# Kernel optimization log

Hardware: AMD Instinct MI355X
Metric: run time of the kernel (lower is better)

Reference implementation:

```python
import math
import jax, jax.numpy as jnp
import numpy as np
from jax import lax


def _l2n(v, eps=1e-12):
    return v / (jnp.linalg.norm(v) + eps)


def _sn(w_bar, u, v):
    # one power iteration (as in SpectralNorm with power_iterations=1)
    h = w_bar.shape[0]
    wm = w_bar.reshape(h, -1)
    v = _l2n(wm.T @ u)
    u = _l2n(wm @ v)
    u = lax.stop_gradient(u)  # u, v are updated via .data in torch (no grad)
    v = lax.stop_gradient(v)
    sigma = u @ (wm @ v)
    return w_bar / sigma


def _conv(x, w, stride, pad):
    return lax.conv_general_dilated(
        x, w, (stride, stride), [(pad, pad), (pad, pad)],
        dimension_numbers=('NCHW', 'OIHW', 'NCHW'))


def _make_blur_kernel():
    k = jnp.array([1., 3., 3., 1.], jnp.float32)
    k2 = k[None, :] * k[:, None]
    return k2 / k2.sum()  # 4x4, sums to 1


def _blur(x, k2, pad):
    # upfirdn2d with up=1, down=1: pad then depthwise FIR filter
    C = x.shape[1]
    xp = jnp.pad(x, ((0, 0), (0, 0), (pad[0], pad[1]), (pad[0], pad[1])))
    w = jnp.tile(k2[None, None], (C, 1, 1, 1))  # [C,1,4,4]
    return lax.conv_general_dilated(
        xp, w, (1, 1), 'VALID', feature_group_count=C,
        dimension_numbers=('NCHW', 'OIHW', 'NCHW'))


def setup_inputs() -> dict:
    key = jax.random.key(0)
    ks = jax.random.split(key, 12)
    Cin, Cout = 256, 512
    x = jax.random.normal(ks[0], (16, Cin, 64, 64), jnp.float32)
    w1_bar = jax.random.normal(ks[1], (Cin, Cin, 3, 3), jnp.float32) * 0.05
    u1 = _l2n(jax.random.normal(ks[2], (Cin,), jnp.float32))
    v1 = _l2n(jax.random.normal(ks[3], (Cin * 9,), jnp.float32))
    b1 = jnp.zeros((Cin,), jnp.float32)
    w2_bar = jax.random.normal(ks[4], (Cout, Cin, 3, 3), jnp.float32) * 0.05
    u2 = _l2n(jax.random.normal(ks[5], (Cout,), jnp.float32))
    v2 = _l2n(jax.random.normal(ks[6], (Cin * 9,), jnp.float32))
    b2 = jnp.zeros((Cout,), jnp.float32)
    ws_bar = jax.random.normal(ks[7], (Cout, Cin, 1, 1), jnp.float32) * 0.05
    us = _l2n(jax.random.normal(ks[8], (Cout,), jnp.float32))
    vs = _l2n(jax.random.normal(ks[9], (Cin,), jnp.float32))
    return dict(x=x, w1_bar=w1_bar, u1=u1, v1=v1, b1=b1,
                w2_bar=w2_bar, u2=u2, v2=v2, b2=b2,
                ws_bar=ws_bar, us=us, vs=vs)


def reference(x, w1_bar, u1, v1, b1, w2_bar, u2, v2, b2, ws_bar, us, vs):
    k2 = _make_blur_kernel()
    # conv1: 3x3 same-res, SN conv + bias + LeakyReLU(0.2)
    out = _conv(x, _sn(w1_bar, u1, v1), 1, 1) + b1[None, :, None, None]
    out = jax.nn.leaky_relu(out, 0.2)
    # conv2: blur pad=(2,2) then 3x3 stride-2 SN conv + bias + LeakyReLU
    out = _blur(out, k2, (2, 2))
    out = _conv(out, _sn(w2_bar, u2, v2), 2, 0) + b2[None, :, None, None]
    out = jax.nn.leaky_relu(out, 0.2)
    # skip: blur pad=(1,1) then 1x1 stride-2 SN conv (no bias, no act)
    skip = _blur(x, k2, (1, 1))
    skip = _conv(skip, _sn(ws_bar, us, vs), 2, 0)
    return (out + skip) / math.sqrt(2)
```

## Files before the change

### kernel.cpp

```cpp
#include <hip/hip_runtime.h>
#include <math.h>

typedef unsigned short u16;
typedef __attribute__((ext_vector_type(8))) unsigned short ushort8;
typedef __attribute__((ext_vector_type(4))) unsigned short u16x4;
typedef __attribute__((ext_vector_type(8))) short short8;
typedef __attribute__((ext_vector_type(4))) float f32x4;

__device__ __forceinline__ float b2f(u16 v) {
    unsigned u = ((unsigned)v) << 16; float f; __builtin_memcpy(&f, &u, 4); return f;
}
__device__ __forceinline__ u16 f2b(float f) {
    unsigned u; __builtin_memcpy(&u, &f, 4);
    u = (u + 0x7fffu + ((u >> 16) & 1u)) >> 16;
    return (u16)u;
}
__device__ __forceinline__ float ldin(const void* p, int i, int flag) {
    return flag ? ((const float*)p)[i] : b2f(((const u16*)p)[i]);
}
__device__ __forceinline__ void split2(float x, u16& h, u16& l) {
    h = f2b(x);
    l = f2b(x - b2f(h));
}
__device__ __forceinline__ ushort8 zero8() {
    ushort8 z;
#pragma unroll
    for (int i = 0; i < 8; ++i) z[i] = 0;
    return z;
}
__device__ __forceinline__ void tile_barrier() {
    asm volatile("s_waitcnt lgkmcnt(0)" ::: "memory");
    __builtin_amdgcn_s_barrier();
    asm volatile("" ::: "memory");
}

__global__ void detect_kernel(const unsigned* __restrict__ xw, int* __restrict__ flag) {
    __shared__ int red[4];
    int tid = threadIdx.x, lane = tid & 63, wid = tid >> 6;
    int cnt = 0;
    for (int i = 0; i < 16; ++i) {
        unsigned w = xw[tid * 16 + i];
        unsigned e = (w >> 23) & 0xFF;
        if (e >= 77u && e <= 157u) ++cnt;
    }
    for (int o = 32; o; o >>= 1) cnt += __shfl_down(cnt, o, 64);
    if (lane == 0) red[wid] = cnt;
    __syncthreads();
    if (tid == 0) flag[0] = (red[0] + red[1] + red[2] + red[3] >= 2048) ? 1 : 0;
}

__global__ void sig_init_kernel(float* __restrict__ t, float* __restrict__ ns) {
    int i = blockIdx.x * 256 + threadIdx.x;
    if (i < 4864) t[i] = 0.f;
    if (i < 3) ns[i] = 0.f;
}

__global__ void sig_t_kernel(const void* __restrict__ w1, const void* __restrict__ u1,
                             const void* __restrict__ w2, const void* __restrict__ u2,
                             const void* __restrict__ wsb, const void* __restrict__ us,
                             const int* __restrict__ flagp, float* __restrict__ t) {
    __shared__ float ush[64];
    int blk = blockIdx.x;
    int flag = flagp[0];
    const void* W; const void* U; int m, toff, jc, ic;
    if (blk < 36)       { W = w1;  U = u1; m = 2304; toff = 0;    jc = blk % 9; ic = blk / 9; }
    else if (blk < 108) { int r = blk - 36;  W = w2;  U = u2; m = 2304; toff = 2304; jc = r % 9; ic = r / 9; }
    else                { int r = blk - 108; W = wsb; U = us; m = 256;  toff = 4608; jc = 0;     ic = r; }
    int tid = threadIdx.x;
    if (tid < 64) ush[tid] = ldin(U, ic * 64 + tid, flag);
    __syncthreads();
    int j = jc * 256 + tid;
    float acc = 0.f;
    int base = ic * 64 * m + j;
    for (int ii = 0; ii < 64; ++ii) acc += ldin(W, base + ii * m, flag) * ush[ii];
    atomicAdd(&t[toff + j], acc);
}

__global__ void sig_norm_kernel(float* __restrict__ t, float* __restrict__ ntinv) {
    __shared__ float red[4];
    int b = blockIdx.x;
    int m = (b == 2) ? 256 : 2304;
    int toff = b * 2304;
    int tid = threadIdx.x, lane = tid & 63, wid = tid >> 6;
    float s = 0.f;
    for (int j = tid; j < m; j += 256) { float v = t[toff + j]; s += v * v; }
    for (int o = 32; o; o >>= 1) s += __shfl_down(s, o, 64);
    if (lane == 0) red[wid] = s;
    __syncthreads();
    if (tid == 0) ntinv[b] = 1.f / (sqrtf(red[0] + red[1] + red[2] + red[3]) + 1e-12f);
}

__global__ void sig_s_kernel(const void* __restrict__ w1, const void* __restrict__ w2,
                             const void* __restrict__ wsb, const int* __restrict__ flagp,
                             const float* __restrict__ t, const float* __restrict__ ntinv,
                             float* __restrict__ ns) {
    int flag = flagp[0];
    int wg = blockIdx.x * 4 + (threadIdx.x >> 6);
    int lane = threadIdx.x & 63;
    const void* W; int m, toff, i, b;
    if (wg < 256)      { W = w1;  m = 2304; toff = 0;    i = wg;       b = 0; }
    else if (wg < 768) { W = w2;  m = 2304; toff = 2304; i = wg - 256; b = 1; }
    else               { W = wsb; m = 256;  toff = 4608; i = wg - 768; b = 2; }
    float acc = 0.f;
    int base = i * m;
    for (int j = lane; j < m; j += 64) acc += ldin(W, base + j, flag) * t[toff + j];
    for (int o = 32; o; o >>= 1) acc += __shfl_down(acc, o, 64);
    if (lane == 0) { float s = acc * ntinv[b]; atomicAdd(&ns[b], s * s); }
}

__global__ void sig_fin_kernel(const float* __restrict__ ns, float* __restrict__ inv_sigma) {
    int b = threadIdx.x;
    if (b < 3) { float s2 = ns[b]; float s = sqrtf(s2); inv_sigma[b] = (s + 1e-12f) / s2; }
}

__global__ void wprep_kernel(const void* __restrict__ w1b, const void* __restrict__ w2b,
                             const void* __restrict__ wsb,
                             const void* __restrict__ b1,  const void* __restrict__ b2,
                             const float* __restrict__ inv_sigma, const int* __restrict__ flagp,
                             u16* __restrict__ w1h, u16* __restrict__ w1l,
                             u16* __restrict__ w2h, u16* __restrict__ w2l,
                             u16* __restrict__ wsh, u16* __restrict__ wsl,
                             float* __restrict__ b1f, float* __restrict__ b2f_) {
    int idx = blockIdx.x * 256 + threadIdx.x;
    int flag = flagp[0];
    float s0 = inv_sigma[0], s1 = inv_sigma[1], s2 = inv_sigma[2];
    if (idx < 589824) {
        int kyx = idx / 65536; int rem = idx - kyx * 65536;
        int co = rem >> 8, ci = rem & 255;
        float w = ldin(w1b, ((co << 8) + ci) * 9 + kyx, flag) * s0;
        split2(w, w1h[idx], w1l[idx]);
    } else if (idx < 589824 + 1179648) {
        int i2 = idx - 589824;
        int kyx = i2 / 131072; int rem = i2 - kyx * 131072;
        int co = rem >> 8, ci = rem & 255;
        float w = ldin(w2b, ((co << 8) + ci) * 9 + kyx, flag) * s1;
        split2(w, w2h[i2], w2l[i2]);
    } else if (idx < 1900544) {
        int i3 = idx - 1769472;
        float w = ldin(wsb, i3, flag) * s2;
        split2(w, wsh[i3], wsl[i3]);
    } else if (idx < 1900544 + 256) {
        b1f[idx - 1900544] = ldin(b1, idx - 1900544, flag);
    } else if (idx < 1900544 + 768) {
        b2f_[idx - 1900800] = ldin(b2, idx - 1900800, flag);
    }
}

__global__ void transpose_kernel(const void* __restrict__ x, u16* __restrict__ xh,
                                 u16* __restrict__ xl,
                                 const int* __restrict__ flagp, int n0) {
    __shared__ float tile[32][65];
    int flag = flagp[0];
    int ny  = blockIdx.x;
    int ci0 = blockIdx.y * 32;
    int nl = ny >> 6, y = ny & 63;
    int t = threadIdx.x;
    int ci_l = t >> 3, x8 = (t & 7) * 8;
    int base = ((n0 + nl) * 256 + ci0 + ci_l) * 4096 + y * 64 + x8;
#pragma unroll
    for (int k = 0; k < 8; ++k) tile[ci_l][x8 + k] = ldin(x, base + k, flag);
    __syncthreads();
    int x_l = t >> 2, oc = (t & 3) * 8;
    size_t o = ((size_t)ny * 64 + x_l) * 256 + ci0 + oc;
    ushort8 h, l;
#pragma unroll
    for (int k = 0; k < 8; ++k) {
        u16 hh, ll; split2(tile[oc + k][x_l], hh, ll);
        h[k] = hh; l[k] = ll;
    }
    *(ushort8*)&xh[o] = h;
    *(ushort8*)&xl[o] = l;
}

__device__ __constant__ float BW[4] = {0.125f, 0.375f, 0.375f, 0.125f};

__global__ void blur1_kernel(const u16* __restrict__ a1h, const u16* __restrict__ a1l,
                             u16* __restrict__ bh, u16* __restrict__ bl) {
    int idx = blockIdx.x * 256 + threadIdx.x;
    int q = (idx & 63) * 4;
    int rem = idx >> 6;
    int xq = rem % 65; rem /= 65;
    int yq = rem % 65;
    int n  = rem / 65;
    float4 acc = {0.f, 0.f, 0.f, 0.f};
#pragma unroll
    for (int i = 0; i < 4; ++i) {
        int yy = yq + i - 2;
        if ((unsigned)yy >= 64u) continue;
#pragma unroll
        for (int j = 0; j < 4; ++j) {
            int xx = xq + j - 2;
            if ((unsigned)xx >= 64u) continue;
            float w = BW[i] * BW[j];
            size_t g = ((size_t)((n * 64 + yy) * 64 + xx) << 8) + q;
            u16x4 vh = *(const u16x4*)&a1h[g];
            u16x4 vl = *(const u16x4*)&a1l[g];
            acc.x += w * (b2f(vh[0]) + b2f(vl[0]));
            acc.y += w * (b2f(vh[1]) + b2f(vl[1]));
            acc.z += w * (b2f(vh[2]) + b2f(vl[2]));
            acc.w += w * (b2f(vh[3]) + b2f(vl[3]));
        }
    }
    u16x4 h, l;
    u16 hh, ll;
    split2(acc.x, hh, ll); h[0] = hh; l[0] = ll;
    split2(acc.y, hh, ll); h[1] = hh; l[1] = ll;
    split2(acc.z, hh, ll); h[2] = hh; l[2] = ll;
    split2(acc.w, hh, ll); h[3] = hh; l[3] = ll;
    *(u16x4*)&bh[(size_t)idx * 4] = h;
    *(u16x4*)&bl[(size_t)idx * 4] = l;
}

__global__ void blursample_kernel(const u16* __restrict__ xh, const u16* __restrict__ xl,
                                  u16* __restrict__ sh, u16* __restrict__ sl) {
    int idx = blockIdx.x * 256 + threadIdx.x;
    int q = (idx & 63) * 4;
    int rem = idx >> 6;
    int xo = rem & 31;
    int yo = (rem >> 5) & 31;
    int n  = rem >> 10;
    float4 acc = {0.f, 0.f, 0.f, 0.f};
#pragma unroll
    for (int i = 0; i < 4; ++i) {
        int yy = 2 * yo + i - 1;
        if ((unsigned)yy >= 64u) continue;
#pragma unroll
        for (int j = 0; j < 4; ++j) {
            int xx = 2 * xo + j - 1;
            if ((unsigned)xx >= 64u) continue;
            float w = BW[i] * BW[j];
            size_t g = ((size_t)((n * 64 + yy) * 64 + xx) << 8) + q;
            u16x4 vh = *(const u16x4*)&xh[g];
            u16x4 vl = *(const u16x4*)&xl[g];
            acc.x += w * (b2f(vh[0]) + b2f(vl[0]));
            acc.y += w * (b2f(vh[1]) + b2f(vl[1]));
            acc.z += w * (b2f(vh[2]) + b2f(vl[2]));
            acc.w += w * (b2f(vh[3]) + b2f(vl[3]));
        }
    }
    u16x4 h, l;
    u16 hh, ll;
    split2(acc.x, hh, ll); h[0] = hh; l[0] = ll;
    split2(acc.y, hh, ll); h[1] = hh; l[1] = ll;
    split2(acc.z, hh, ll); h[2] = hh; l[2] = ll;
    split2(acc.w, hh, ll); h[3] = hh; l[3] = ll;
    *(u16x4*)&sh[(size_t)idx * 4] = h;
    *(u16x4*)&sl[(size_t)idx * 4] = l;
}

#define LDK 40

#define C1_LOAD(IT, RAH0, RAH1, RAL0, RAL1, RBH0, RBH1, RBL0, RBL1) {          \
    int p_ = (IT) >> 3, kc_ = (IT) & 7;                                        \
    const u16* wh_ = w1h + (size_t)p_ * 65536;                                 \
    const u16* wl_ = w1l + (size_t)p_ * 65536;                                 \
    size_t gs_ = (size_t)(co_base + ra) * 256 + kc_ * 32 + ka;                 \
    RAH0 = *(const ushort8*)&wh_[gs_];                                         \
    RAH1 = *(const ushort8*)&wh_[gs_ + 8];                                     \
    if (DOLO) { RAL0 = *(const ushort8*)&wl_[gs_];                             \
                RAL1 = *(const ushort8*)&wl_[gs_ + 8]; }                       \
    int dy_ = p_ / 3 - 1, dx_ = p_ % 3 - 1;                                    \
    int yy_ = y0 + (ra >> 6) + dy_, xx_ = (ra & 63) + dx_;                     \
    if ((unsigned)yy_ < 64u && (unsigned)xx_ < 64u) {                          \
        size_t g_ = ((size_t)((n * 64 + yy_) * 64 + xx_) << 8) + kc_ * 32 + ka;\
        RBH0 = *(const ushort8*)&xh[g_];                                       \
        RBH1 = *(const ushort8*)&xh[g_ + 8];                                   \
        if (DOLO) { RBL0 = *(const ushort8*)&xl[g_];                           \
                    RBL1 = *(const ushort8*)&xl[g_ + 8]; }                     \
    } else {                                                                   \
        RBH0 = zero8(); RBH1 = zero8();                                        \
        if (DOLO) { RBL0 = zero8(); RBL1 = zero8(); }                          \
    }                                                                          \
}

template <bool DOLO>
__device__ __forceinline__ void conv1_body(
        const u16* __restrict__ xh, const u16* __restrict__ xl,
        const u16* __restrict__ w1h, const u16* __restrict__ w1l,
        const float* __restrict__ b1f, u16* __restrict__ a1h, u16* __restrict__ a1l,
        u16* Ah, u16* Al, u16* Bh, u16* Bl) {
    int tid = threadIdx.x, lane = tid & 63, wid = tid >> 6;
    int col = lane & 15, quad = lane >> 4;
    int wco = (wid >> 1) * 64, wsp = (wid & 1) * 64;
    int bidx = blockIdx.x;
    int sp_blk = (bidx & 7) * 32 + (bidx >> 3);
    int sp_base = sp_blk * 128;
    int co_base = blockIdx.y * 128;
    int n  = sp_base >> 12;
    int y0 = (sp_base & 4095) >> 6;
    int ra = tid >> 1, ka = (tid & 1) * 16;

    f32x4 acc[4][4];
#pragma unroll
    for (int i = 0; i < 4; ++i)
#pragma unroll
        for (int j = 0; j < 4; ++j) acc[i][j] = (f32x4){0.f, 0.f, 0.f, 0.f};

    ushort8 nAh0, nAh1, nAl0, nAl1, nBh0, nBh1, nBl0, nBl1;
    C1_LOAD(0, nAh0, nAh1, nAl0, nAl1, nBh0, nBh1, nBl0, nBl1);

    for (int it = 0; it < 72; ++it) {
        __syncthreads();
        *(ushort8*)&Ah[ra * LDK + ka]     = nAh0;
        *(ushort8*)&Ah[ra * LDK + ka + 8] = nAh1;
        if (DOLO) {
            *(ushort8*)&Al[ra * LDK + ka]     = nAl0;
            *(ushort8*)&Al[ra * LDK + ka + 8] = nAl1;
        }
        *(ushort8*)&Bh[ra * LDK + ka]     = nBh0;
        *(ushort8*)&Bh[ra * LDK + ka + 8] = nBh1;
        if (DOLO) {
            *(ushort8*)&Bl[ra * LDK + ka]     = nBl0;
            *(ushort8*)&Bl[ra * LDK + ka + 8] = nBl1;
        }
        int itn = (it + 1 < 72) ? it + 1 : it;
        C1_LOAD(itn, nAh0, nAh1, nAl0, nAl1, nBh0, nBh1, nBl0, nBl1);
        tile_barrier();
        short8 ah[4], al[4];
#pragma unroll
        for (int tm = 0; tm < 4; ++tm) {
            ah[tm] = *(const short8*)&Ah[(wco + tm * 16 + col) * LDK + quad * 8];
            if (DOLO) al[tm] = *(const short8*)&Al[(wco + tm * 16 + col) * LDK + quad * 8];
        }
#pragma unroll
        for (int tn = 0; tn < 4; ++tn) {
            short8 bh = *(const short8*)&Bh[(wsp + tn * 16 + col) * LDK + quad * 8];
            short8 bl;
            if (DOLO) bl = *(const short8*)&Bl[(wsp + tn * 16 + col) * LDK + quad * 8];
#pragma unroll
            for (int tm = 0; tm < 4; ++tm) {
                acc[tm][tn] = __builtin_amdgcn_mfma_f32_16x16x32_bf16(ah[tm], bh, acc[tm][tn], 0, 0, 0);
                if (DOLO) {
                    acc[tm][tn] = __builtin_amdgcn_mfma_f32_16x16x32_bf16(ah[tm], bl, acc[tm][tn], 0, 0, 0);
                    acc[tm][tn] = __builtin_amdgcn_mfma_f32_16x16x32_bf16(al[tm], bh, acc[tm][tn], 0, 0, 0);
                }
            }
        }
    }
#pragma unroll
    for (int tm = 0; tm < 4; ++tm) {
        int cog = co_base + wco + tm * 16 + quad * 4;
        float4 bias = *(const float4*)&b1f[cog];
        float bb[4] = {bias.x, bias.y, bias.z, bias.w};
#pragma unroll
        for (int tn = 0; tn < 4; ++tn) {
            int sp = sp_base + wsp + tn * 16 + col;
            u16x4 oh, ol;
#pragma unroll
            for (int r = 0; r < 4; ++r) {
                float v = acc[tm][tn][r] + bb[r];
                v = v > 0.f ? v : 0.2f * v;
                u16 hh, ll; split2(v, hh, ll);
                oh[r] = hh; ol[r] = ll;
            }
            *(u16x4*)&a1h[((size_t)sp << 8) + cog] = oh;
            *(u16x4*)&a1l[((size_t)sp << 8) + cog] = ol;
        }
    }
}

__global__ __launch_bounds__(256, 2) void conv1_kernel(
        const u16* __restrict__ xh, const u16* __restrict__ xl,
        const u16* __restrict__ w1h, const u16* __restrict__ w1l,
        const float* __restrict__ b1f, u16* __restrict__ a1h, u16* __restrict__ a1l,
        const int* __restrict__ flagp) {
    __shared__ u16 Ah[128 * LDK];
    __shared__ u16 Al[128 * LDK];
    __shared__ u16 Bh[128 * LDK];
    __shared__ u16 Bl[128 * LDK];
    if (flagp[0]) conv1_body<true >(xh, xl, w1h, w1l, b1f, a1h, a1l, Ah, Al, Bh, Bl);
    else          conv1_body<false>(xh, xl, w1h, w1l, b1f, a1h, a1l, Ah, Al, Bh, Bl);
}

#define C2_LOAD(IT, RAH, RAL, RBH0, RBH1, RBL0, RBL1) {                        \
    int p_ = (IT) >> 3, kc_ = (IT) & 7; int ci0_ = kc_ * 32;                   \
    const u16* wh_ = (p_ < 9) ? w2h + (size_t)p_ * 131072 : wsh;               \
    const u16* wl_ = (p_ < 9) ? w2l + (size_t)p_ * 131072 : wsl;               \
    size_t gs_ = (size_t)(co_base + ra) * 256 + ci0_ + ka;                     \
    RAH = *(const ushort8*)&wh_[gs_];                                          \
    if (DOLO) RAL = *(const ushort8*)&wl_[gs_];                                \
    const u16 *sh_, *sl_; size_t g_;                                           \
    if (p_ < 9) {                                                              \
        int ky_ = p_ / 3, kx_ = p_ % 3;                                        \
        int yi_ = 2 * (yo0 + (r_st >> 5)) + ky_;                               \
        int xi_ = 2 * (r_st & 31) + kx_;                                       \
        g_ = (size_t)((n * 65 + yi_) * 65 + xi_) * 256 + ci0_ + k_st;          \
        sh_ = bl1h; sl_ = bl1l;                                                \
    } else {                                                                   \
        g_ = ((size_t)(sp_base + r_st) << 8) + ci0_ + k_st;                    \
        sh_ = skh; sl_ = skl;                                                  \
    }                                                                          \
    RBH0 = *(const ushort8*)&sh_[g_];                                          \
    RBH1 = *(const ushort8*)&sh_[g_ + 8];                                      \
    if (DOLO) { RBL0 = *(const ushort8*)&sl_[g_];                              \
                RBL1 = *(const ushort8*)&sl_[g_ + 8]; }                        \
}

template <bool DOLO>
__device__ __forceinline__ void conv2_body(
        const u16* __restrict__ bl1h, const u16* __restrict__ bl1l,
        const u16* __restrict__ skh,  const u16* __restrict__ skl,
        const u16* __restrict__ w2h, const u16* __restrict__ w2l,
        const u16* __restrict__ wsh, const u16* __restrict__ wsl,
        const float* __restrict__ b2f_, void* __restrict__ out, int n0,
        u16* Ah, u16* Al, u16* Bh, u16* Bl, int flag) {
    int tid = threadIdx.x, lane = tid & 63, wid = tid >> 6;
    int col = lane & 15, quad = lane >> 4;
    int wco = (wid >> 1) * 32, wsp = (wid & 1) * 64;
    int b = blockIdx.x;
    int img    = b & 7;
    int r      = b >> 3;
    int co_blk = r & 7;
    int sp_in  = r >> 3;
    int sp_base = img * 1024 + sp_in * 128;
    int co_base = co_blk * 64;
    int n   = img;
    int yo0 = sp_in * 4;
    int r_st = tid >> 1, k_st = (tid & 1) * 16;
    int ra = tid >> 2, ka = (tid & 3) * 8;

    f32x4 acc[2][4], accs[2][4];
#pragma unroll
    for (int i = 0; i < 2; ++i)
#pragma unroll
        for (int j = 0; j < 4; ++j) {
            acc[i][j]  = (f32x4){0.f, 0.f, 0.f, 0.f};
            accs[i][j] = (f32x4){0.f, 0.f, 0.f, 0.f};
        }

    ushort8 nAh, nAl, nBh0, nBh1, nBl0, nBl1;
    C2_LOAD(0, nAh, nAl, nBh0, nBh1, nBl0, nBl1);

    for (int it = 0; it < 80; ++it) {
        int p = it >> 3;
        __syncthreads();
        *(ushort8*)&Ah[ra * LDK + ka] = nAh;
        if (DOLO) *(ushort8*)&Al[ra * LDK + ka] = nAl;
        *(ushort8*)&Bh[r_st * LDK + k_st]     = nBh0;
        *(ushort8*)&Bh[r_st * LDK + k_st + 8] = nBh1;
        if (DOLO) {
            *(ushort8*)&Bl[r_st * LDK + k_st]     = nBl0;
            *(ushort8*)&Bl[r_st * LDK + k_st + 8] = nBl1;
        }
        int itn = (it + 1 < 80) ? it + 1 : it;
        C2_LOAD(itn, nAh, nAl, nBh0, nBh1, nBl0, nBl1);
        tile_barrier();
        short8 ah[2], al[2];
#pragma unroll
        for (int tm = 0; tm < 2; ++tm) {
            ah[tm] = *(const short8*)&Ah[(wco + tm * 16 + col) * LDK + quad * 8];
            if (DOLO) al[tm] = *(const short8*)&Al[(wco + tm * 16 + col) * LDK + quad * 8];
        }
        if (p < 9) {
#pragma unroll
            for (int tn = 0; tn < 4; ++tn) {
                short8 bh = *(const short8*)&Bh[(wsp + tn * 16 + col) * LDK + quad * 8];
                short8 bl;
                if (DOLO) bl = *(const short8*)&Bl[(wsp + tn * 16 + col) * LDK + quad * 8];
#pragma unroll
                for (int tm = 0; tm < 2; ++tm) {
                    acc[tm][tn] = __builtin_amdgcn_mfma_f32_16x16x32_bf16(ah[tm], bh, acc[tm][tn], 0, 0, 0);
                    if (DOLO) {
                        acc[tm][tn] = __builtin_amdgcn_mfma_f32_16x16x32_bf16(ah[tm], bl, acc[tm][tn], 0, 0, 0);
                        acc[tm][tn] = __builtin_amdgcn_mfma_f32_16x16x32_bf16(al[tm], bh, acc[tm][tn], 0, 0, 0);
                    }
                }
            }
        } else {
#pragma unroll
            for (int tn = 0; tn < 4; ++tn) {
                short8 bh = *(const short8*)&Bh[(wsp + tn * 16 + col) * LDK + quad * 8];
                short8 bl;
                if (DOLO) bl = *(const short8*)&Bl[(wsp + tn * 16 + col) * LDK + quad * 8];
#pragma unroll
                for (int tm = 0; tm < 2; ++tm) {
                    accs[tm][tn] = __builtin_amdgcn_mfma_f32_16x16x32_bf16(ah[tm], bh, accs[tm][tn], 0, 0, 0);
                    if (DOLO) {
                        accs[tm][tn] = __builtin_amdgcn_mfma_f32_16x16x32_bf16(ah[tm], bl, accs[tm][tn], 0, 0, 0);
                        accs[tm][tn] = __builtin_amdgcn_mfma_f32_16x16x32_bf16(al[tm], bh, accs[tm][tn], 0, 0, 0);
                    }
                }
            }
        }
    }
    const float RS2 = 0.70710678118654752f;
#pragma unroll
    for (int tm = 0; tm < 2; ++tm) {
        int cog = co_base + wco + tm * 16 + quad * 4;
        float4 bias = *(const float4*)&b2f_[cog];
        float bb[4] = {bias.x, bias.y, bias.z, bias.w};
#pragma unroll
        for (int tn = 0; tn < 4; ++tn) {
            int sp  = sp_base + wsp + tn * 16 + col;
            int ng  = n0 + (sp >> 10);
            int rem = sp & 1023;
            size_t ob = ((size_t)ng * 512 + cog) * 1024 + rem;
#pragma unroll
            for (int r = 0; r < 4; ++r) {
                float v = acc[tm][tn][r] + bb[r];
                v = v > 0.f ? v : 0.2f * v;
                v = (v + accs[tm][tn][r]) * RS2;
                if (flag) ((float*)out)[ob + (size_t)r * 1024] = v;
                else      ((u16*)out)[ob + (size_t)r * 1024]   = f2b(v);
            }
        }
    }
}

__global__ __launch_bounds__(256, 2) void conv2_kernel(
        const u16* __restrict__ bl1h, const u16* __restrict__ bl1l,
        const u16* __restrict__ skh,  const u16* __restrict__ skl,
        const u16* __restrict__ w2h, const u16* __restrict__ w2l,
        const u16* __restrict__ wsh, const u16* __restrict__ wsl,
        const float* __restrict__ b2f_, const int* __restrict__ flagp,
        void* __restrict__ out, int n0) {
    __shared__ u16 Ah[64 * LDK];
    __shared__ u16 Al[64 * LDK];
    __shared__ u16 Bh[128 * LDK];
    __shared__ u16 Bl[128 * LDK];
    int flag = flagp[0];
    if (flag) conv2_body<true >(bl1h, bl1l, skh, skl, w2h, w2l, wsh, wsl, b2f_, out, n0, Ah, Al, Bh, Bl, flag);
    else      conv2_body<false>(bl1h, bl1l, skh, skl, w2h, w2l, wsh, wsl, b2f_, out, n0, Ah, Al, Bh, Bl, flag);
}

extern "C" void kernel_launch(void* const* d_in, const int* in_sizes, int n_in,
                              void* d_out, int out_size, void* d_ws, size_t ws_size,
                              hipStream_t stream) {
    const void* x   = d_in[0];
    const void* w1b = d_in[1];
    const void* u1  = d_in[2];
    const void* b1  = d_in[4];
    const void* w2b = d_in[5];
    const void* u2  = d_in[6];
    const void* b2  = d_in[8];
    const void* wsb = d_in[9];
    const void* us  = d_in[10];

    char* ws = (char*)d_ws;
    int*   flag      = (int*)(ws);
    float* inv_sigma = (float*)(ws + 64);
    float* b1f       = (float*)(ws + 1024);
    float* b2fp      = (float*)(ws + 2048);
    u16* w1h = (u16*)(ws + 4096);
    u16* w1l = (u16*)(ws + 1183744);
    u16* w2h = (u16*)(ws + 2363392);
    u16* w2l = (u16*)(ws + 4722688);
    u16* wsh = (u16*)(ws + 7081984);
    u16* wsl = (u16*)(ws + 7344128);
    u16* xth  = (u16*)(ws + 7606272);
    u16* xtl  = (u16*)(ws + 7606272 + 16777216);
    u16* bl1h = (u16*)(ws + 7606272);
    u16* bl1l = (u16*)(ws + 7606272 + 17305600);
    u16* a1h = (u16*)(ws + 42217472);
    u16* a1l = (u16*)(ws + 42217472 + 16777216);
    u16* skh = (u16*)(ws + 75771904);
    u16* skl = (u16*)(ws + 75771904 + 4194304);
    float* tvec  = (float*)(ws + 7606272);
    float* ntinv = (float*)(ws + 7606272 + 19456);
    float* ns    = (float*)(ws + 7606272 + 19520);

    detect_kernel<<<1, 256, 0, stream>>>((const unsigned*)x, flag);
    sig_init_kernel<<<19, 256, 0, stream>>>(tvec, ns);
    sig_t_kernel<<<116, 256, 0, stream>>>(w1b, u1, w2b, u2, wsb, us, flag, tvec);
    sig_norm_kernel<<<3, 256, 0, stream>>>(tvec, ntinv);
    sig_s_kernel<<<320, 256, 0, stream>>>(w1b, w2b, wsb, flag, tvec, ntinv, ns);
    sig_fin_kernel<<<1, 64, 0, stream>>>(ns, inv_sigma);
    wprep_kernel<<<7427, 256, 0, stream>>>(w1b, w2b, wsb, b1, b2, inv_sigma, flag,
                                           w1h, w1l, w2h, w2l, wsh, wsl, b1f, b2fp);
    for (int c = 0; c < 2; ++c) {
        int n0 = c * 8;
        transpose_kernel<<<dim3(512, 8), 256, 0, stream>>>(x, xth, xtl, flag, n0);
        blursample_kernel<<<2048, 256, 0, stream>>>(xth, xtl, skh, skl);
        conv1_kernel<<<dim3(256, 2), 256, 0, stream>>>(xth, xtl, w1h, w1l, b1f, a1h, a1l, flag);
        blur1_kernel<<<8450, 256, 0, stream>>>(a1h, a1l, bl1h, bl1l);
        conv2_kernel<<<512, 256, 0, stream>>>(bl1h, bl1l, skh, skl, w2h, w2l,
                                              wsh, wsl, b2fp, flag, d_out, n0);
    }
}
```

Measured before the change: 703.7 us.

## Load weight fragments directly from global into registers, bypassing LDS

Both conv kernels stop staging the weight (A) tiles through shared memory. Each wave now loads its own MFMA A-fragments straight from global memory into a double-buffered register array, prefetched one iteration ahead, and the K loop is unrolled by two so the buffers can be indexed statically. This removes LDS writes and reads for weights and shrinks LDS use. In exchange it adds redundant global/L2 traffic, since waves sharing output channels each fetch the same weights, and raises register pressure.

```diff
diff --git a/kernel.cpp b/kernel.cpp
--- a/kernel.cpp
+++ b/kernel.cpp
@@ -250,15 +250,8 @@
 
 #define LDK 40
 
-#define C1_LOAD(IT, RAH0, RAH1, RAL0, RAL1, RBH0, RBH1, RBL0, RBL1) {          \
+#define C1_LOADB(IT, RBH0, RBH1, RBL0, RBL1) {                                 \
     int p_ = (IT) >> 3, kc_ = (IT) & 7;                                        \
-    const u16* wh_ = w1h + (size_t)p_ * 65536;                                 \
-    const u16* wl_ = w1l + (size_t)p_ * 65536;                                 \
-    size_t gs_ = (size_t)(co_base + ra) * 256 + kc_ * 32 + ka;                 \
-    RAH0 = *(const ushort8*)&wh_[gs_];                                         \
-    RAH1 = *(const ushort8*)&wh_[gs_ + 8];                                     \
-    if (DOLO) { RAL0 = *(const ushort8*)&wl_[gs_];                             \
-                RAL1 = *(const ushort8*)&wl_[gs_ + 8]; }                       \
     int dy_ = p_ / 3 - 1, dx_ = p_ % 3 - 1;                                    \
     int yy_ = y0 + (ra >> 6) + dy_, xx_ = (ra & 63) + dx_;                     \
     if ((unsigned)yy_ < 64u && (unsigned)xx_ < 64u) {                          \
@@ -273,12 +266,25 @@
     }                                                                          \
 }
 
+#define C1_LOADA(IT, AH, AL) {                                                 \
+    int p_ = (IT) >> 3, kc_ = (IT) & 7;                                        \
+    const u16* wh_ = w1h + (size_t)p_ * 65536;                                 \
+    const u16* wl_ = w1l + (size_t)p_ * 65536;                                 \
+    _Pragma("unroll")                                                          \
+    for (int tm_ = 0; tm_ < 4; ++tm_) {                                        \
+        size_t a_ = (size_t)(co_base + wco + tm_ * 16 + col) * 256             \
+                    + kc_ * 32 + quad * 8;                                     \
+        AH[tm_] = *(const ushort8*)&wh_[a_];                                   \
+        if (DOLO) AL[tm_] = *(const ushort8*)&wl_[a_];                         \
+    }                                                                          \
+}
+
 template <bool DOLO>
 __device__ __forceinline__ void conv1_body(
         const u16* __restrict__ xh, const u16* __restrict__ xl,
         const u16* __restrict__ w1h, const u16* __restrict__ w1l,
         const float* __restrict__ b1f, u16* __restrict__ a1h, u16* __restrict__ a1l,
-        u16* Ah, u16* Al, u16* Bh, u16* Bl) {
+        u16* Bh, u16* Bl) {
     int tid = threadIdx.x, lane = tid & 63, wid = tid >> 6;
     int col = lane & 15, quad = lane >> 4;
     int wco = (wid >> 1) * 64, wsp = (wid & 1) * 64;
@@ -296,43 +302,41 @@
 #pragma unroll
         for (int j = 0; j < 4; ++j) acc[i][j] = (f32x4){0.f, 0.f, 0.f, 0.f};
 
-    ushort8 nAh0, nAh1, nAl0, nAl1, nBh0, nBh1, nBl0, nBl1;
-    C1_LOAD(0, nAh0, nAh1, nAl0, nAl1, nBh0, nBh1, nBl0, nBl1);
-
-    for (int it = 0; it < 72; ++it) {
-        __syncthreads();
-        *(ushort8*)&Ah[ra * LDK + ka]     = nAh0;
-        *(ushort8*)&Ah[ra * LDK + ka + 8] = nAh1;
-        if (DOLO) {
-            *(ushort8*)&Al[ra * LDK + ka]     = nAl0;
-            *(ushort8*)&Al[ra * LDK + ka + 8] = nAl1;
-        }
-        *(ushort8*)&Bh[ra * LDK + ka]     = nBh0;
-        *(ushort8*)&Bh[ra * LDK + ka + 8] = nBh1;
-        if (DOLO) {
-            *(ushort8*)&Bl[ra * LDK + ka]     = nBl0;
-            *(ushort8*)&Bl[ra * LDK + ka + 8] = nBl1;
-        }
-        int itn = (it + 1 < 72) ? it + 1 : it;
-        C1_LOAD(itn, nAh0, nAh1, nAl0, nAl1, nBh0, nBh1, nBl0, nBl1);
-        tile_barrier();
-        short8 ah[4], al[4];
-#pragma unroll
-        for (int tm = 0; tm < 4; ++tm) {
-            ah[tm] = *(const short8*)&Ah[(wco + tm * 16 + col) * LDK + quad * 8];
-            if (DOLO) al[tm] = *(const short8*)&Al[(wco + tm * 16 + col) * LDK + quad * 8];
-        }
-#pragma unroll
-        for (int tn = 0; tn < 4; ++tn) {
-            short8 bh = *(const short8*)&Bh[(wsp + tn * 16 + col) * LDK + quad * 8];
-            short8 bl;
-            if (DOLO) bl = *(const short8*)&Bl[(wsp + tn * 16 + col) * LDK + quad * 8];
-#pragma unroll
-            for (int tm = 0; tm < 4; ++tm) {
-                acc[tm][tn] = __builtin_amdgcn_mfma_f32_16x16x32_bf16(ah[tm], bh, acc[tm][tn], 0, 0, 0);
-                if (DOLO) {
-                    acc[tm][tn] = __builtin_amdgcn_mfma_f32_16x16x32_bf16(ah[tm], bl, acc[tm][tn], 0, 0, 0);
-                    acc[tm][tn] = __builtin_amdgcn_mfma_f32_16x16x32_bf16(al[tm], bh, acc[tm][tn], 0, 0, 0);
+    ushort8 nBh0, nBh1, nBl0, nBl1;
+    ushort8 Af[2][4], Alf[2][4];
+    C1_LOADB(0, nBh0, nBh1, nBl0, nBl1);
+    C1_LOADA(0, Af[0], Alf[0]);
+
+    for (int itb = 0; itb < 72; itb += 2) {
+#pragma unroll
+        for (int u = 0; u < 2; ++u) {
+            int it = itb + u;
+            __syncthreads();
+            *(ushort8*)&Bh[ra * LDK + ka]     = nBh0;
+            *(ushort8*)&Bh[ra * LDK + ka + 8] = nBh1;
+            if (DOLO) {
+                *(ushort8*)&Bl[ra * LDK + ka]     = nBl0;
+                *(ushort8*)&Bl[ra * LDK + ka + 8] = nBl1;
+            }
+            int itn = (it + 1 < 72) ? it + 1 : it;
+            C1_LOADB(itn, nBh0, nBh1, nBl0, nBl1);
+            tile_barrier();
+            C1_LOADA(itn, Af[u ^ 1], Alf[u ^ 1]);
+#pragma unroll
+            for (int tn = 0; tn < 4; ++tn) {
+                short8 bh = *(const short8*)&Bh[(wsp + tn * 16 + col) * LDK + quad * 8];
+                short8 bl;
+                if (DOLO) bl = *(const short8*)&Bl[(wsp + tn * 16 + col) * LDK + quad * 8];
+#pragma unroll
+                for (int tm = 0; tm < 4; ++tm) {
+                    short8 ah, al;
+                    __builtin_memcpy(&ah, &Af[u][tm], 16);
+                    if (DOLO) __builtin_memcpy(&al, &Alf[u][tm], 16);
+                    acc[tm][tn] = __builtin_amdgcn_mfma_f32_16x16x32_bf16(ah, bh, acc[tm][tn], 0, 0, 0);
+                    if (DOLO) {
+                        acc[tm][tn] = __builtin_amdgcn_mfma_f32_16x16x32_bf16(ah, bl, acc[tm][tn], 0, 0, 0);
+                        acc[tm][tn] = __builtin_amdgcn_mfma_f32_16x16x32_bf16(al, bh, acc[tm][tn], 0, 0, 0);
+                    }
                 }
             }
         }
@@ -364,21 +368,14 @@
         const u16* __restrict__ w1h, const u16* __restrict__ w1l,
         const float* __restrict__ b1f, u16* __restrict__ a1h, u16* __restrict__ a1l,
         const int* __restrict__ flagp) {
-    __shared__ u16 Ah[128 * LDK];
-    __shared__ u16 Al[128 * LDK];
     __shared__ u16 Bh[128 * LDK];
     __shared__ u16 Bl[128 * LDK];
-    if (flagp[0]) conv1_body<true >(xh, xl, w1h, w1l, b1f, a1h, a1l, Ah, Al, Bh, Bl);
-    else          conv1_body<false>(xh, xl, w1h, w1l, b1f, a1h, a1l, Ah, Al, Bh, Bl);
-}
-
-#define C2_LOAD(IT, RAH, RAL, RBH0, RBH1, RBL0, RBL1) {                        \
+    if (flagp[0]) conv1_body<true >(xh, xl, w1h, w1l, b1f, a1h, a1l, Bh, Bl);
+    else          conv1_body<false>(xh, xl, w1h, w1l, b1f, a1h, a1l, Bh, Bl);
+}
+
+#define C2_LOADB(IT, RBH0, RBH1, RBL0, RBL1) {                                 \
     int p_ = (IT) >> 3, kc_ = (IT) & 7; int ci0_ = kc_ * 32;                   \
-    const u16* wh_ = (p_ < 9) ? w2h + (size_t)p_ * 131072 : wsh;               \
-    const u16* wl_ = (p_ < 9) ? w2l + (size_t)p_ * 131072 : wsl;               \
-    size_t gs_ = (size_t)(co_base + ra) * 256 + ci0_ + ka;                     \
-    RAH = *(const ushort8*)&wh_[gs_];                                          \
-    if (DOLO) RAL = *(const ushort8*)&wl_[gs_];                                \
     const u16 *sh_, *sl_; size_t g_;                                           \
     if (p_ < 9) {                                                              \
         int ky_ = p_ / 3, kx_ = p_ % 3;                                        \
@@ -396,6 +393,19 @@
                 RBL1 = *(const ushort8*)&sl_[g_ + 8]; }                        \
 }
 
+#define C2_LOADA(IT, AH, AL) {                                                 \
+    int p_ = (IT) >> 3, kc_ = (IT) & 7; int ci0_ = kc_ * 32;                   \
+    const u16* wh_ = (p_ < 9) ? w2h + (size_t)p_ * 131072 : wsh;               \
+    const u16* wl_ = (p_ < 9) ? w2l + (size_t)p_ * 131072 : wsl;               \
+    _Pragma("unroll")                                                          \
+    for (int tm_ = 0; tm_ < 2; ++tm_) {                                        \
+        size_t a_ = (size_t)(co_base + wco + tm_ * 16 + col) * 256             \
+                    + ci0_ + quad * 8;                                         \
+        AH[tm_] = *(const ushort8*)&wh_[a_];                                   \
+        if (DOLO) AL[tm_] = *(const ushort8*)&wl_[a_];                         \
+    }                                                                          \
+}
+
 template <bool DOLO>
 __device__ __forceinline__ void conv2_body(
         const u16* __restrict__ bl1h, const u16* __restrict__ bl1l,
@@ -403,7 +413,7 @@
         const u16* __restrict__ w2h, const u16* __restrict__ w2l,
         const u16* __restrict__ wsh, const u16* __restrict__ wsl,
         const float* __restrict__ b2f_, void* __restrict__ out, int n0,
-        u16* Ah, u16* Al, u16* Bh, u16* Bl, int flag) {
+        u16* Bh, u16* Bl, int flag) {
     int tid = threadIdx.x, lane = tid & 63, wid = tid >> 6;
     int col = lane & 15, quad = lane >> 4;
     int wco = (wid >> 1) * 32, wsp = (wid & 1) * 64;
@@ -417,7 +427,6 @@
     int n   = img;
     int yo0 = sp_in * 4;
     int r_st = tid >> 1, k_st = (tid & 1) * 16;
-    int ra = tid >> 2, ka = (tid & 3) * 8;
 
     f32x4 acc[2][4], accs[2][4];
 #pragma unroll
@@ -428,30 +437,28 @@
             accs[i][j] = (f32x4){0.f, 0.f, 0.f, 0.f};
         }
 
-    ushort8 nAh, nAl, nBh0, nBh1, nBl0, nBl1;
-    C2_LOAD(0, nAh, nAl, nBh0, nBh1, nBl0, nBl1);
-
-    for (int it = 0; it < 80; ++it) {
-        int p = it >> 3;
-        __syncthreads();
-        *(ushort8*)&Ah[ra * LDK + ka] = nAh;
-        if (DOLO) *(ushort8*)&Al[ra * LDK + ka] = nAl;
-        *(ushort8*)&Bh[r_st * LDK + k_st]     = nBh0;
-        *(ushort8*)&Bh[r_st * LDK + k_st + 8] = nBh1;
-        if (DOLO) {
-            *(ushort8*)&Bl[r_st * LDK + k_st]     = nBl0;
-            *(ushort8*)&Bl[r_st * LDK + k_st + 8] = nBl1;
-        }
-        int itn = (it + 1 < 80) ? it + 1 : it;
-        C2_LOAD(itn, nAh, nAl, nBh0, nBh1, nBl0, nBl1);
-        tile_barrier();
-        short8 ah[2], al[2];
-#pragma unroll
-        for (int tm = 0; tm < 2; ++tm) {
-            ah[tm] = *(const short8*)&Ah[(wco + tm * 16 + col) * LDK + quad * 8];
-            if (DOLO) al[tm] = *(const short8*)&Al[(wco + tm * 16 + col) * LDK + quad * 8];
-        }
-        if (p < 9) {
+    ushort8 nBh0, nBh1, nBl0, nBl1;
+    ushort8 Af[2][2], Alf[2][2];
+    C2_LOADB(0, nBh0, nBh1, nBl0, nBl1);
+    C2_LOADA(0, Af[0], Alf[0]);
+
+    for (int itb = 0; itb < 80; itb += 2) {
+#pragma unroll
+        for (int u = 0; u < 2; ++u) {
+            int it = itb + u;
+            int p = it >> 3;
+            __syncthreads();
+            *(ushort8*)&Bh[r_st * LDK + k_st]     = nBh0;
+            *(ushort8*)&Bh[r_st * LDK + k_st + 8] = nBh1;
+            if (DOLO) {
+                *(ushort8*)&Bl[r_st * LDK + k_st]     = nBl0;
+                *(ushort8*)&Bl[r_st * LDK + k_st + 8] = nBl1;
+            }
+            int itn = (it + 1 < 80) ? it + 1 : it;
+            C2_LOADB(itn, nBh0, nBh1, nBl0, nBl1);
+            tile_barrier();
+            C2_LOADA(itn, Af[u ^ 1], Alf[u ^ 1]);
+            f32x4 (*ac)[4] = (p < 9) ? acc : accs;
 #pragma unroll
             for (int tn = 0; tn < 4; ++tn) {
                 short8 bh = *(const short8*)&Bh[(wsp + tn * 16 + col) * LDK + quad * 8];
@@ -459,25 +466,13 @@
                 if (DOLO) bl = *(const short8*)&Bl[(wsp + tn * 16 + col) * LDK + quad * 8];
 #pragma unroll
                 for (int tm = 0; tm < 2; ++tm) {
-                    acc[tm][tn] = __builtin_amdgcn_mfma_f32_16x16x32_bf16(ah[tm], bh, acc[tm][tn], 0, 0, 0);
+                    short8 ah, al;
+                    __builtin_memcpy(&ah, &Af[u][tm], 16);
+                    if (DOLO) __builtin_memcpy(&al, &Alf[u][tm], 16);
+                    ac[tm][tn] = __builtin_amdgcn_mfma_f32_16x16x32_bf16(ah, bh, ac[tm][tn], 0, 0, 0);
                     if (DOLO) {
-                        acc[tm][tn] = __builtin_amdgcn_mfma_f32_16x16x32_bf16(ah[tm], bl, acc[tm][tn], 0, 0, 0);
-                        acc[tm][tn] = __builtin_amdgcn_mfma_f32_16x16x32_bf16(al[tm], bh, acc[tm][tn], 0, 0, 0);
-                    }
-                }
-            }
-        } else {
-#pragma unroll
-            for (int tn = 0; tn < 4; ++tn) {
-                short8 bh = *(const short8*)&Bh[(wsp + tn * 16 + col) * LDK + quad * 8];
-                short8 bl;
-                if (DOLO) bl = *(const short8*)&Bl[(wsp + tn * 16 + col) * LDK + quad * 8];
-#pragma unroll
-                for (int tm = 0; tm < 2; ++tm) {
-                    accs[tm][tn] = __builtin_amdgcn_mfma_f32_16x16x32_bf16(ah[tm], bh, accs[tm][tn], 0, 0, 0);
-                    if (DOLO) {
-                        accs[tm][tn] = __builtin_amdgcn_mfma_f32_16x16x32_bf16(ah[tm], bl, accs[tm][tn], 0, 0, 0);
-                        accs[tm][tn] = __builtin_amdgcn_mfma_f32_16x16x32_bf16(al[tm], bh, accs[tm][tn], 0, 0, 0);
+                        ac[tm][tn] = __builtin_amdgcn_mfma_f32_16x16x32_bf16(ah, bl, ac[tm][tn], 0, 0, 0);
+                        ac[tm][tn] = __builtin_amdgcn_mfma_f32_16x16x32_bf16(al, bh, ac[tm][tn], 0, 0, 0);
                     }
                 }
             }
@@ -496,12 +491,12 @@
             int rem = sp & 1023;
             size_t ob = ((size_t)ng * 512 + cog) * 1024 + rem;
 #pragma unroll
-            for (int r = 0; r < 4; ++r) {
-                float v = acc[tm][tn][r] + bb[r];
+            for (int r2 = 0; r2 < 4; ++r2) {
+                float v = acc[tm][tn][r2] + bb[r2];
                 v = v > 0.f ? v : 0.2f * v;
-                v = (v + accs[tm][tn][r]) * RS2;
-                if (flag) ((float*)out)[ob + (size_t)r * 1024] = v;
-                else      ((u16*)out)[ob + (size_t)r * 1024]   = f2b(v);
+                v = (v + accs[tm][tn][r2]) * RS2;
+                if (flag) ((float*)out)[ob + (size_t)r2 * 1024] = v;
+                else      ((u16*)out)[ob + (size_t)r2 * 1024]   = f2b(v);
             }
         }
     }
@@ -514,13 +509,11 @@
         const u16* __restrict__ wsh, const u16* __restrict__ wsl,
         const float* __restrict__ b2f_, const int* __restrict__ flagp,
         void* __restrict__ out, int n0) {
-    __shared__ u16 Ah[64 * LDK];
-    __shared__ u16 Al[64 * LDK];
     __shared__ u16 Bh[128 * LDK];
     __shared__ u16 Bl[128 * LDK];
     int flag = flagp[0];
-    if (flag) conv2_body<true >(bl1h, bl1l, skh, skl, w2h, w2l, wsh, wsl, b2f_, out, n0, Ah, Al, Bh, Bl, flag);
-    else      conv2_body<false>(bl1h, bl1l, skh, skl, w2h, w2l, wsh, wsl, b2f_, out, n0, Ah, Al, Bh, Bl, flag);
+    if (flag) conv2_body<true >(bl1h, bl1l, skh, skl, w2h, w2l, wsh, wsl, b2f_, out, n0, Bh, Bl, flag);
+    else      conv2_body<false>(bl1h, bl1l, skh, skl, w2h, w2l, wsh, wsl, b2f_, out, n0, Bh, Bl, flag);
 }
 
 extern "C" void kernel_launch(void* const* d_in, const int* in_sizes, int n_in,
```

Measured after the change: 890.8 us. 1.27x slower.
